# Optimization experiments

Measured on AMD Instinct MI355X. Metric: run time of the kernel, lower is better.

## Reference

```python
import jax, jax.numpy as jnp
import numpy as np

D = 256      # d_model
NH = 8       # heads
NL = 3       # layers
DFF = 1024   # ffn hidden
WIN = 64     # attention window
EPS = 1e-5


def _sin_pos_embed(L, d):
    # Sinusoidal positional embedding, matches _create_pos_embedding.
    pos = jnp.arange(L, dtype=jnp.float32)[:, None]
    div = jnp.exp(jnp.arange(0, d, 2, dtype=jnp.float32) * (-np.log(10000.0) / d))
    pe = jnp.zeros((L, d), jnp.float32)
    pe = pe.at[:, 0::2].set(jnp.sin(pos * div))
    pe = pe.at[:, 1::2].set(jnp.cos(pos * div))
    return pe  # [L, D]


def _layer_norm(x, scale, bias):
    m = jnp.mean(x, axis=-1, keepdims=True)
    v = jnp.mean(jnp.square(x - m), axis=-1, keepdims=True)
    return (x - m) * jax.lax.rsqrt(v + EPS) * scale + bias


def _mha(x, Wi, bi, Wo, bo):
    # x: [N, S, D]; Wi: [3D, D]; Wo: [D, D]. torch nn.MultiheadAttention semantics (eval, no dropout).
    N, S, _ = x.shape
    dh = D // NH
    qkv = x @ Wi.T + bi                       # [N, S, 3D]
    q, k, v = jnp.split(qkv, 3, axis=-1)
    q = q.reshape(N, S, NH, dh).transpose(0, 2, 1, 3) * (dh ** -0.5)
    k = k.reshape(N, S, NH, dh).transpose(0, 2, 1, 3)
    v = v.reshape(N, S, NH, dh).transpose(0, 2, 1, 3)
    attn = jax.nn.softmax(jnp.einsum('nhqd,nhkd->nhqk', q, k), axis=-1)
    out = jnp.einsum('nhqk,nhkd->nhqd', attn, v)
    out = out.transpose(0, 2, 1, 3).reshape(N, S, D)
    return out @ Wo.T + bo


def setup_inputs() -> dict:
    key = jax.random.key(0)
    ks = jax.random.split(key, 16)
    s = 0.02
    return {
        'features': jax.random.normal(ks[0], (32, D, 32, 32), jnp.float32),
        'in_proj_w': jax.random.normal(ks[1], (NL, 3 * D, D), jnp.float32) * s,
        'in_proj_b': jnp.zeros((NL, 3 * D), jnp.float32),
        'out_proj_w': jax.random.normal(ks[2], (NL, D, D), jnp.float32) * s,
        'out_proj_b': jnp.zeros((NL, D), jnp.float32),
        'w1': jax.random.normal(ks[3], (NL, DFF, D), jnp.float32) * s,
        'b1': jnp.zeros((NL, DFF), jnp.float32),
        'w2': jax.random.normal(ks[4], (NL, D, DFF), jnp.float32) * s,
        'b2': jnp.zeros((NL, D), jnp.float32),
        'ln1_s': jnp.ones((NL, D), jnp.float32),
        'ln1_b': jnp.zeros((NL, D), jnp.float32),
        'ln2_s': jnp.ones((NL, D), jnp.float32),
        'ln2_b': jnp.zeros((NL, D), jnp.float32),
        'fnorm_s': jnp.ones((D,), jnp.float32),
        'fnorm_b': jnp.zeros((D,), jnp.float32),
    }


def reference(features, in_proj_w, in_proj_b, out_proj_w, out_proj_b,
              w1, b1, w2, b2, ln1_s, ln1_b, ln2_s, ln2_b, fnorm_s, fnorm_b):
    B, C, H, W = features.shape
    L = H * W
    x = features.reshape(B, C, L).transpose(0, 2, 1)   # [B, L, D]
    x = x + _sin_pos_embed(L, D)[None]                 # L == 1024 == max_len, no interp
    nw = L // WIN                                      # non-overlapping windows
    for i in range(NL):
        # windowed self-attention: all windows batched in one MHA call
        xw = x.reshape(B * nw, WIN, D)
        att = _mha(xw, in_proj_w[i], in_proj_b[i], out_proj_w[i], out_proj_b[i])
        att = att.reshape(B, L, D)
        x = _layer_norm(x + att, ln1_s[i], ln1_b[i])
        h = jax.nn.gelu(x @ w1[i].T + b1[i], approximate=False) @ w2[i].T + b2[i]
        x = _layer_norm(x + h, ln2_s[i], ln2_b[i])
    x = _layer_norm(x, fnorm_s, fnorm_b)
    return x.transpose(0, 2, 1).reshape(B, C, H, W)
```

## Files before the change

kernel.cpp:

```cpp
#include <hip/hip_runtime.h>
#include <hip/hip_bf16.h>

#define BSZ 32
#define DM 256
#define LSEQ 1024
#define MTOK (BSZ * LSEQ)
#define NHEAD 8
#define DHEAD 32
#define WIN 64
#define DFF 1024
#define M8 ((size_t)MTOK * 8)

typedef short bf16x8 __attribute__((ext_vector_type(8)));
typedef float f32x4 __attribute__((ext_vector_type(4)));
typedef unsigned short u16x8 __attribute__((ext_vector_type(8)));

union BF { __hip_bfloat16 h; unsigned short u; };
__device__ __forceinline__ unsigned short f2bf(float f) { BF b; b.h = __float2bfloat16(f); return b.u; }
__device__ __forceinline__ float bf2f(unsigned short u) { return __uint_as_float((unsigned)u << 16); }

#define GLD_LDS16(gp, lp) __builtin_amdgcn_global_load_lds( \
    (const __attribute__((address_space(1))) void*)(gp),    \
    (__attribute__((address_space(3))) void*)(lp), 16, 0, 0)

__device__ __forceinline__ float gelu_fast(float x) {
    float t = x * (0.7978845608f + 0.0356774081f * x * x);
    return x / (1.0f + __expf(-2.0f * t));
}

__global__ __launch_bounds__(256) void cvt_kernel(
    const float* __restrict__ s, unsigned short* __restrict__ d,
    int N, int K, int nl)
{
    int K8 = K >> 3;
    int per = N * K8;
    int c = blockIdx.x * 256 + threadIdx.x;
    if (c >= per * nl) return;
    int layer = c / per, rem = c - layer * per;
    int n = rem / K8, kc = rem - n * K8;
    const float* sp = s + (size_t)layer * N * K + (size_t)n * K + kc * 8;
    float4 v0 = *(const float4*)sp, v1 = *(const float4*)(sp + 4);
    uint4 o;
    o.x = f2bf(v0.x) | ((unsigned)f2bf(v0.y) << 16);
    o.y = f2bf(v0.z) | ((unsigned)f2bf(v0.w) << 16);
    o.z = f2bf(v1.x) | ((unsigned)f2bf(v1.y) << 16);
    o.w = f2bf(v1.z) | ((unsigned)f2bf(v1.w) << 16);
    *(uint4*)(d + (size_t)layer * N * K + (size_t)kc * N * 8 + (size_t)n * 8) = o;
}

__global__ __launch_bounds__(256) void pe_kernel(float* __restrict__ PE)
{
    int l = blockIdx.x, c = threadIdx.x;
    int i2 = c & ~1;
    float div = expf(-9.210340371976184f * (float)i2 / 256.0f);
    float ang = (float)l * div;
    PE[l * DM + c] = (c & 1) ? cosf(ang) : sinf(ang);
}

__global__ __launch_bounds__(256) void embed_kernel(
    const float* __restrict__ F, const float* __restrict__ PE,
    float* __restrict__ Xf, unsigned short* __restrict__ Xb)
{
    __shared__ float tile[64][65];
    int b = blockIdx.z, l0 = blockIdx.y * 64, c0 = blockIdx.x * 64;
    int tid = threadIdx.x;
    int li = tid & 63, c4 = tid >> 6;
    #pragma unroll
    for (int it = 0; it < 16; ++it) {
        int c = c4 + it * 4;
        tile[c][li] = F[((size_t)(b * DM + c0 + c)) * LSEQ + l0 + li];
    }
    __syncthreads();
    int ci = tid & 63, l4 = tid >> 6;
    #pragma unroll
    for (int it = 0; it < 16; ++it) {
        int l = l4 + it * 4;
        float x = tile[ci][l] + PE[(l0 + l) * DM + c0 + ci];
        Xf[((size_t)b * LSEQ + l0 + l) * DM + c0 + ci] = x;
    }
    int ch = tid >> 5;
    int lx = tid & 31;
    #pragma unroll
    for (int rd = 0; rd < 2; ++rd) {
        int l = lx + rd * 32;
        unsigned short vs[8];
        #pragma unroll
        for (int e = 0; e < 8; ++e) {
            int c = ch * 8 + e;
            vs[e] = f2bf(tile[c][l] + PE[(l0 + l) * DM + c0 + c]);
        }
        uint4 o;
        o.x = vs[0] | ((unsigned)vs[1] << 16);
        o.y = vs[2] | ((unsigned)vs[3] << 16);
        o.z = vs[4] | ((unsigned)vs[5] << 16);
        o.w = vs[6] | ((unsigned)vs[7] << 16);
        *(uint4*)(Xb + ((size_t)((c0 >> 3) + ch)) * M8 +
                  (size_t)(b * LSEQ + l0 + l) * 8) = o;
    }
}

__global__ __launch_bounds__(256) void gemm_mfma_kernel(
    const unsigned short* __restrict__ A, const unsigned short* __restrict__ Bw,
    const float* __restrict__ bias, unsigned short* __restrict__ Cb,
    int M, int N, int K, int gelu)
{
    __shared__ __align__(16) char smem[17408];
    const int tid = threadIdx.x;
    const int lane = tid & 63, wave = tid >> 6;
    const int l15 = lane & 15, quad = lane >> 4;
    const int wm = (wave & 1) * 64, wn = (wave >> 1) * 64;
    const int m0 = blockIdx.x * 128, n0 = blockIdx.y * 128;
    const size_t Ma8 = (size_t)M * 8, Nb8 = (size_t)N * 8;
    const size_t astep = 4 * Ma8, bstep = 4 * Nb8;

    const unsigned short* ap[4];
    const unsigned short* bp[4];
    #pragma unroll
    for (int i = 0; i < 4; ++i)
        ap[i] = A + quad * Ma8 + (size_t)(m0 + wm + i * 16 + l15) * 8;
    #pragma unroll
    for (int j = 0; j < 4; ++j)
        bp[j] = Bw + quad * Nb8 + (size_t)(n0 + wn + j * 16 + l15) * 8;

    f32x4 acc[4][4] = {};
    bf16x8 aA[4], bA[4], aB[4], bB[4];
    #pragma unroll
    for (int i = 0; i < 4; ++i) aA[i] = *(const bf16x8*)(ap[i]);
    #pragma unroll
    for (int j = 0; j < 4; ++j) bA[j] = *(const bf16x8*)(bp[j]);

    const int iters = K >> 5;
    for (int t = 0; t < iters; t += 2) {
        size_t o1 = (size_t)(t + 1);
        #pragma unroll
        for (int i = 0; i < 4; ++i) aB[i] = *(const bf16x8*)(ap[i] + o1 * astep);
        #pragma unroll
        for (int j = 0; j < 4; ++j) bB[j] = *(const bf16x8*)(bp[j] + o1 * bstep);
        #pragma unroll
        for (int i = 0; i < 4; ++i)
            #pragma unroll
            for (int j = 0; j < 4; ++j)
                acc[i][j] = __builtin_amdgcn_mfma_f32_16x16x32_bf16(
                    aA[i], bA[j], acc[i][j], 0, 0, 0);
        size_t o2 = (size_t)((t + 2 < iters) ? t + 2 : iters - 1);
        #pragma unroll
        for (int i = 0; i < 4; ++i) aA[i] = *(const bf16x8*)(ap[i] + o2 * astep);
        #pragma unroll
        for (int j = 0; j < 4; ++j) bA[j] = *(const bf16x8*)(bp[j] + o2 * bstep);
        #pragma unroll
        for (int i = 0; i < 4; ++i)
            #pragma unroll
            for (int j = 0; j < 4; ++j)
                acc[i][j] = __builtin_amdgcn_mfma_f32_16x16x32_bf16(
                    aB[i], bB[j], acc[i][j], 0, 0, 0);
    }

    float* Es = (float*)(smem + wave * 4352);
    const int r16 = lane >> 2;
    const int cg  = (lane & 3) * 16;
    #pragma unroll
    for (int i = 0; i < 4; ++i) {
        #pragma unroll
        for (int j = 0; j < 4; ++j)
            #pragma unroll
            for (int r = 0; r < 4; ++r)
                Es[(quad * 4 + r) * 68 + j * 16 + l15] = acc[i][j][r];
        asm volatile("s_waitcnt lgkmcnt(0)" ::: "memory");

        int m = m0 + wm + i * 16 + r16;
        int nb = n0 + wn + cg;
        float v[16];
        #pragma unroll
        for (int c = 0; c < 4; ++c) {
            f32x4 t = *(const f32x4*)&Es[r16 * 68 + cg + c * 4];
            v[c * 4 + 0] = t[0]; v[c * 4 + 1] = t[1];
            v[c * 4 + 2] = t[2]; v[c * 4 + 3] = t[3];
        }
        #pragma unroll
        for (int c = 0; c < 4; ++c) {
            float4 bb = *(const float4*)(bias + nb + c * 4);
            v[c * 4 + 0] += bb.x; v[c * 4 + 1] += bb.y;
            v[c * 4 + 2] += bb.z; v[c * 4 + 3] += bb.w;
        }
        if (gelu) {
            #pragma unroll
            for (int e = 0; e < 16; ++e) v[e] = gelu_fast(v[e]);
        }
        size_t gb = ((size_t)(nb >> 3)) * Ma8 + (size_t)m * 8;
        #pragma unroll
        for (int c = 0; c < 2; ++c) {
            uint4 o;
            o.x = f2bf(v[c * 8 + 0]) | ((unsigned)f2bf(v[c * 8 + 1]) << 16);
            o.y = f2bf(v[c * 8 + 2]) | ((unsigned)f2bf(v[c * 8 + 3]) << 16);
            o.z = f2bf(v[c * 8 + 4]) | ((unsigned)f2bf(v[c * 8 + 5]) << 16);
            o.w = f2bf(v[c * 8 + 6]) | ((unsigned)f2bf(v[c * 8 + 7]) << 16);
            *(uint4*)(Cb + gb + (size_t)c * Ma8) = o;
        }
        asm volatile("" ::: "memory");
    }
}

__global__ __launch_bounds__(256) void gemm_ln_kernel(
    const unsigned short* __restrict__ A, const unsigned short* __restrict__ Bw,
    const float* __restrict__ bias, const float* __restrict__ resid,
    const float* __restrict__ lns, const float* __restrict__ lnb,
    float* __restrict__ Xf, unsigned short* __restrict__ Xb, int K)
{
    __shared__ __align__(16) char smem[17408];
    __shared__ float Ss[256], Sq[256];
    const int tid = threadIdx.x;
    const int lane = tid & 63, wave = tid >> 6;
    const int l15 = lane & 15, quad = lane >> 4;
    const int wn = wave * 64;
    const int m0 = blockIdx.x * 64;
    const size_t Nb8 = (size_t)DM * 8;
    const size_t astep = 4 * M8, bstep = 4 * Nb8;

    const unsigned short* ap[4];
    const unsigned short* bp[4];
    #pragma unroll
    for (int i = 0; i < 4; ++i)
        ap[i] = A + quad * M8 + (size_t)(m0 + i * 16 + l15) * 8;
    #pragma unroll
    for (int j = 0; j < 4; ++j)
        bp[j] = Bw + quad * Nb8 + (size_t)(wn + j * 16 + l15) * 8;

    f32x4 acc[4][4] = {};
    bf16x8 aA[4], bA[4], aB[4], bB[4];
    #pragma unroll
    for (int i = 0; i < 4; ++i) aA[i] = *(const bf16x8*)(ap[i]);
    #pragma unroll
    for (int j = 0; j < 4; ++j) bA[j] = *(const bf16x8*)(bp[j]);

    const int iters = K >> 5;
    for (int t = 0; t < iters; t += 2) {
        size_t o1 = (size_t)(t + 1);
        #pragma unroll
        for (int i = 0; i < 4; ++i) aB[i] = *(const bf16x8*)(ap[i] + o1 * astep);
        #pragma unroll
        for (int j = 0; j < 4; ++j) bB[j] = *(const bf16x8*)(bp[j] + o1 * bstep);
        #pragma unroll
        for (int i = 0; i < 4; ++i)
            #pragma unroll
            for (int j = 0; j < 4; ++j)
                acc[i][j] = __builtin_amdgcn_mfma_f32_16x16x32_bf16(
                    aA[i], bA[j], acc[i][j], 0, 0, 0);
        size_t o2 = (size_t)((t + 2 < iters) ? t + 2 : iters - 1);
        #pragma unroll
        for (int i = 0; i < 4; ++i) aA[i] = *(const bf16x8*)(ap[i] + o2 * astep);
        #pragma unroll
        for (int j = 0; j < 4; ++j) bA[j] = *(const bf16x8*)(bp[j] + o2 * bstep);
        #pragma unroll
        for (int i = 0; i < 4; ++i)
            #pragma unroll
            for (int j = 0; j < 4; ++j)
                acc[i][j] = __builtin_amdgcn_mfma_f32_16x16x32_bf16(
                    aB[i], bB[j], acc[i][j], 0, 0, 0);
    }

    float bj[4], scj[4], bbj[4];
    #pragma unroll
    for (int j = 0; j < 4; ++j) {
        int col = wn + j * 16 + l15;
        bj[j] = bias[col]; scj[j] = lns[col]; bbj[j] = lnb[col];
    }
    #pragma unroll
    for (int i = 0; i < 4; ++i)
        #pragma unroll
        for (int r = 0; r < 4; ++r) {
            const float* rp = resid + (size_t)(m0 + i * 16 + quad * 4 + r) * DM + wn;
            #pragma unroll
            for (int j = 0; j < 4; ++j)
                acc[i][j][r] += bj[j] + rp[j * 16 + l15];
        }

    #pragma unroll
    for (int i = 0; i < 4; ++i)
        #pragma unroll
        for (int r = 0; r < 4; ++r) {
            float s = 0.f, q = 0.f;
            #pragma unroll
            for (int j = 0; j < 4; ++j) {
                float x = acc[i][j][r];
                s += x; q = fmaf(x, x, q);
            }
            #pragma unroll
            for (int off = 1; off < 16; off <<= 1) {
                s += __shfl_xor(s, off);
                q += __shfl_xor(q, off);
            }
            if (l15 == 0) {
                int row = i * 16 + quad * 4 + r;
                Ss[wave * 64 + row] = s;
                Sq[wave * 64 + row] = q;
            }
        }
    __syncthreads();
    #pragma unroll
    for (int i = 0; i < 4; ++i)
        #pragma unroll
        for (int r = 0; r < 4; ++r) {
            int row = i * 16 + quad * 4 + r;
            float s = Ss[row] + Ss[64 + row] + Ss[128 + row] + Ss[192 + row];
            float q = Sq[row] + Sq[64 + row] + Sq[128 + row] + Sq[192 + row];
            float mean = s * (1.0f / 256.0f);
            float var  = q * (1.0f / 256.0f) - mean * mean;
            float rinv = rsqrtf(var + 1e-5f);
            #pragma unroll
            for (int j = 0; j < 4; ++j)
                acc[i][j][r] = (acc[i][j][r] - mean) * rinv * scj[j] + bbj[j];
        }

    float* Es = (float*)(smem + wave * 4352);
    const int r16 = lane >> 2;
    const int cg  = (lane & 3) * 16;
    #pragma unroll
    for (int i = 0; i < 4; ++i) {
        #pragma unroll
        for (int j = 0; j < 4; ++j)
            #pragma unroll
            for (int r = 0; r < 4; ++r)
                Es[(quad * 4 + r) * 68 + j * 16 + l15] = acc[i][j][r];
        asm volatile("s_waitcnt lgkmcnt(0)" ::: "memory");

        int m = m0 + i * 16 + r16;
        float v[16];
        #pragma unroll
        for (int c = 0; c < 4; ++c) {
            f32x4 t = *(const f32x4*)&Es[r16 * 68 + cg + c * 4];
            v[c * 4 + 0] = t[0]; v[c * 4 + 1] = t[1];
            v[c * 4 + 2] = t[2]; v[c * 4 + 3] = t[3];
        }
        size_t gf = (size_t)m * DM + wn + cg;
        #pragma unroll
        for (int c = 0; c < 4; ++c) {
            float4 o = { v[c * 4 + 0], v[c * 4 + 1], v[c * 4 + 2], v[c * 4 + 3] };
            *(float4*)(Xf + gf + c * 4) = o;
        }
        size_t gb = ((size_t)((wn + cg) >> 3)) * M8 + (size_t)m * 8;
        #pragma unroll
        for (int c = 0; c < 2; ++c) {
            uint4 o;
            o.x = f2bf(v[c * 8 + 0]) | ((unsigned)f2bf(v[c * 8 + 1]) << 16);
            o.y = f2bf(v[c * 8 + 2]) | ((unsigned)f2bf(v[c * 8 + 3]) << 16);
            o.z = f2bf(v[c * 8 + 4]) | ((unsigned)f2bf(v[c * 8 + 5]) << 16);
            o.w = f2bf(v[c * 8 + 6]) | ((unsigned)f2bf(v[c * 8 + 7]) << 16);
            *(uint4*)(Xb + gb + (size_t)c * M8) = o;
        }
        asm volatile("" ::: "memory");
    }
}

__global__ __launch_bounds__(64) void attn_mfma_kernel(
    const unsigned short* __restrict__ QKV, unsigned short* __restrict__ ATT)
{
    __shared__ __align__(16) char smem[22016];
    unsigned short* Qs = (unsigned short*)smem;
    unsigned short* Ks = (unsigned short*)(smem + 4096);
    unsigned short* VT = (unsigned short*)(smem + 8192);
    unsigned short* Ps = (unsigned short*)(smem + 12800);
    float*          Po = (float*)(smem + 12800);

    const int wg = blockIdx.x, h = blockIdx.y;
    const int base = wg * WIN;
    const int lane = threadIdx.x;
    const int l15 = lane & 15, quad = lane >> 4;
    const float scale = 0.17677669529663687f;

    #pragma unroll
    for (int dc = 0; dc < 4; ++dc) {
        GLD_LDS16(QKV + ((size_t)(h * 4 + dc)) * M8 + (size_t)(base + lane) * 8,
                  Qs + dc * 512 + (size_t)lane * 8);
        GLD_LDS16(QKV + ((size_t)(32 + h * 4 + dc)) * M8 + (size_t)(base + lane) * 8,
                  Ks + dc * 512 + (size_t)lane * 8);
    }
    u16x8 vv[4];
    #pragma unroll
    for (int cc = 0; cc < 4; ++cc)
        vv[cc] = *(const u16x8*)(QKV + ((size_t)(64 + h * 4 + cc)) * M8 +
                                 (size_t)(base + lane) * 8);
    #pragma unroll
    for (int cc = 0; cc < 4; ++cc)
        #pragma unroll
        for (int e = 0; e < 8; ++e)
            VT[(cc * 8 + e) * 72 + lane] = vv[cc][e];
    __syncthreads();

    const f32x4 zero4 = {0.f, 0.f, 0.f, 0.f};
    bf16x8 aq[4], bk[4];
    #pragma unroll
    for (int i = 0; i < 4; ++i)
        aq[i] = *(const bf16x8*)(Qs + quad * 512 + (i * 16 + l15) * 8);
    #pragma unroll
    for (int j = 0; j < 4; ++j)
        bk[j] = *(const bf16x8*)(Ks + quad * 512 + (j * 16 + l15) * 8);
    f32x4 S[4][4];
    #pragma unroll
    for (int i = 0; i < 4; ++i)
        #pragma unroll
        for (int j = 0; j < 4; ++j)
            S[i][j] = __builtin_amdgcn_mfma_f32_16x16x32_bf16(aq[i], bk[j], zero4, 0, 0, 0);

    float mx[4][4], sum[4][4];
    #pragma unroll
    for (int i = 0; i < 4; ++i)
        #pragma unroll
        for (int r = 0; r < 4; ++r) {
            float m0 = -1e30f;
            #pragma unroll
            for (int j = 0; j < 4; ++j) {
                S[i][j][r] *= scale;
                m0 = fmaxf(m0, S[i][j][r]);
            }
            mx[i][r] = m0;
        }
    #pragma unroll
    for (int off = 1; off < 16; off <<= 1)
        #pragma unroll
        for (int i = 0; i < 4; ++i)
            #pragma unroll
            for (int r = 0; r < 4; ++r)
                mx[i][r] = fmaxf(mx[i][r], __shfl_xor(mx[i][r], off));
    #pragma unroll
    for (int i = 0; i < 4; ++i)
        #pragma unroll
        for (int r = 0; r < 4; ++r) {
            float s0 = 0.f;
            #pragma unroll
            for (int j = 0; j < 4; ++j) {
                float e = __expf(S[i][j][r] - mx[i][r]);
                S[i][j][r] = e;
                s0 += e;
            }
            sum[i][r] = s0;
        }
    #pragma unroll
    for (int off = 1; off < 16; off <<= 1)
        #pragma unroll
        for (int i = 0; i < 4; ++i)
            #pragma unroll
            for (int r = 0; r < 4; ++r)
                sum[i][r] += __shfl_xor(sum[i][r], off);

    #pragma unroll
    for (int i = 0; i < 4; ++i)
        #pragma unroll
        for (int r = 0; r < 4; ++r) {
            float inv = 1.0f / sum[i][r];
            #pragma unroll
            for (int j = 0; j < 4; ++j)
                Ps[(i * 16 + quad * 4 + r) * 72 + j * 16 + l15] =
                    f2bf(S[i][j][r] * inv);
        }
    asm volatile("s_waitcnt lgkmcnt(0)" ::: "memory");

    bf16x8 ap0[4], ap1[4], bv0[2], bv1[2];
    #pragma unroll
    for (int i = 0; i < 4; ++i) {
        ap0[i] = *(const bf16x8*)(Ps + (i * 16 + l15) * 72 + quad * 8);
        ap1[i] = *(const bf16x8*)(Ps + (i * 16 + l15) * 72 + 32 + quad * 8);
    }
    #pragma unroll
    for (int jd = 0; jd < 2; ++jd) {
        bv0[jd] = *(const bf16x8*)(VT + (jd * 16 + l15) * 72 + quad * 8);
        bv1[jd] = *(const bf16x8*)(VT + (jd * 16 + l15) * 72 + 32 + quad * 8);
    }
    f32x4 O[4][2];
    #pragma unroll
    for (int i = 0; i < 4; ++i)
        #pragma unroll
        for (int jd = 0; jd < 2; ++jd) {
            f32x4 t = __builtin_amdgcn_mfma_f32_16x16x32_bf16(ap0[i], bv0[jd], zero4, 0, 0, 0);
            O[i][jd] = __builtin_amdgcn_mfma_f32_16x16x32_bf16(ap1[i], bv1[jd], t, 0, 0, 0);
        }
    asm volatile("s_waitcnt lgkmcnt(0)" ::: "memory");

    #pragma unroll
    for (int i = 0; i < 4; ++i)
        #pragma unroll
        for (int jd = 0; jd < 2; ++jd)
            #pragma unroll
            for (int r = 0; r < 4; ++r)
                Po[(i * 16 + quad * 4 + r) * 36 + jd * 16 + l15] = O[i][jd][r];
    asm volatile("s_waitcnt lgkmcnt(0)" ::: "memory");

    #pragma unroll
    for (int g = 0; g < 4; ++g) {
        f32x4 t0 = *(const f32x4*)(Po + lane * 36 + g * 8);
        f32x4 t1 = *(const f32x4*)(Po + lane * 36 + g * 8 + 4);
        uint4 w;
        w.x = f2bf(t0[0]) | ((unsigned)f2bf(t0[1]) << 16);
        w.y = f2bf(t0[2]) | ((unsigned)f2bf(t0[3]) << 16);
        w.z = f2bf(t1[0]) | ((unsigned)f2bf(t1[1]) << 16);
        w.w = f2bf(t1[2]) | ((unsigned)f2bf(t1[3]) << 16);
        *(uint4*)(ATT + ((size_t)(h * 4 + g)) * M8 + (size_t)(base + lane) * 8) = w;
    }
}

__global__ __launch_bounds__(256) void out_ln_kernel(
    const float* __restrict__ Xf, const float* __restrict__ sc,
    const float* __restrict__ bi, float* __restrict__ out)
{
    __shared__ float tile[64][257];
    __shared__ float mean_s[64], rinv_s[64];
    int b = blockIdx.y, l0 = blockIdx.x * 64;
    int tid = threadIdx.x, wave = tid >> 6, lane = tid & 63;
    int c = lane * 4;
    #pragma unroll
    for (int it = 0; it < 16; ++it) {
        int tl = wave * 16 + it;
        float4 v = *(const float4*)(Xf + ((size_t)(b * LSEQ + l0 + tl)) * DM + c);
        *(float4*)&tile[tl][c] = v;
        float sm = v.x + v.y + v.z + v.w;
        float sq = v.x * v.x + v.y * v.y + v.z * v.z + v.w * v.w;
        #pragma unroll
        for (int off = 32; off > 0; off >>= 1) {
            sm += __shfl_down(sm, off);
            sq += __shfl_down(sq, off);
        }
        if (lane == 0) {
            float mean = sm * (1.0f / 256.0f);
            float var  = sq * (1.0f / 256.0f) - mean * mean;
            mean_s[tl] = mean;
            rinv_s[tl] = rsqrtf(var + 1e-5f);
        }
    }
    __syncthreads();
    int lout = tid & 63, crow = tid >> 6;
    #pragma unroll
    for (int ct = 0; ct < 4; ++ct) {
        int c0 = ct * 64;
        #pragma unroll
        for (int it = 0; it < 16; ++it) {
            int cc = c0 + crow + it * 4;
            float v = tile[lout][cc];
            out[((size_t)(b * DM + cc)) * LSEQ + l0 + lout] =
                (v - mean_s[lout]) * rinv_s[lout] * sc[cc] + bi[cc];
        }
    }
}

extern "C" void kernel_launch(void* const* d_in, const int* in_sizes, int n_in,
                              void* d_out, int out_size, void* d_ws, size_t ws_size,
                              hipStream_t stream)
{
    const float* F   = (const float*)d_in[0];
    const float* Wi  = (const float*)d_in[1];
    const float* Bi  = (const float*)d_in[2];
    const float* Wo  = (const float*)d_in[3];
    const float* Bo  = (const float*)d_in[4];
    const float* W1  = (const float*)d_in[5];
    const float* B1  = (const float*)d_in[6];
    const float* W2  = (const float*)d_in[7];
    const float* B2  = (const float*)d_in[8];
    const float* L1s = (const float*)d_in[9];
    const float* L1b = (const float*)d_in[10];
    const float* L2s = (const float*)d_in[11];
    const float* L2b = (const float*)d_in[12];
    const float* Fs  = (const float*)d_in[13];
    const float* Fb  = (const float*)d_in[14];

    char* w = (char*)d_ws;
    float*          Xf   = (float*)w;
    unsigned short* QKVb = (unsigned short*)(w + 33554432);
    unsigned short* Hb   = (unsigned short*)(w + 83886080);
    unsigned short* Xb   = (unsigned short*)(w + 150994944);
    unsigned short* ATTb = (unsigned short*)(w + 167772160);
    unsigned short* WB   = (unsigned short*)(w + 184549376);
    float*          PE   = (float*)(w + 189267968);
    unsigned short* Wib  = WB;
    unsigned short* Wob  = WB + 589824;
    unsigned short* W1b  = WB + 786432;
    unsigned short* W2b  = WB + 1572864;

    cvt_kernel<<<(3 * 768 * 32 + 255) / 256, 256, 0, stream>>>(Wi, Wib, 768, 256, 3);
    cvt_kernel<<<(3 * 256 * 32 + 255) / 256, 256, 0, stream>>>(Wo, Wob, 256, 256, 3);
    cvt_kernel<<<(3 * 1024 * 32 + 255) / 256, 256, 0, stream>>>(W1, W1b, 1024, 256, 3);
    cvt_kernel<<<(3 * 256 * 128 + 255) / 256, 256, 0, stream>>>(W2, W2b, 256, 1024, 3);
    pe_kernel<<<LSEQ, 256, 0, stream>>>(PE);
    embed_kernel<<<dim3(DM / 64, LSEQ / 64, BSZ), 256, 0, stream>>>(F, PE, Xf, Xb);

    for (int i = 0; i < 3; ++i) {
        gemm_mfma_kernel<<<dim3(MTOK / 128, 768 / 128), 256, 0, stream>>>(
            Xb, Wib + (size_t)i * 196608, Bi + i * 768, QKVb, MTOK, 768, DM, 0);
        attn_mfma_kernel<<<dim3(BSZ * (LSEQ / WIN), NHEAD), 64, 0, stream>>>(QKVb, ATTb);
        gemm_ln_kernel<<<MTOK / 64, 256, 0, stream>>>(
            ATTb, Wob + (size_t)i * 65536, Bo + i * DM, Xf,
            L1s + i * DM, L1b + i * DM, Xf, Xb, DM);
        gemm_mfma_kernel<<<dim3(MTOK / 128, DFF / 128), 256, 0, stream>>>(
            Xb, W1b + (size_t)i * 262144, B1 + i * DFF, Hb, MTOK, DFF, DM, 1);
        gemm_ln_kernel<<<MTOK / 64, 256, 0, stream>>>(
            Hb, W2b + (size_t)i * 262144, B2 + i * DM, Xf,
            L2s + i * DM, L2b + i * DM, Xf, Xb, DFF);
    }

    out_ln_kernel<<<dim3(LSEQ / 64, BSZ), 256, 0, stream>>>(
        Xf, Fs, Fb, (float*)d_out);
}
```

Baseline: 648.6 us.

## Fuse FFN up-projection, GELU, down-projection and LayerNorm into one kernel

Replaces the separate W1 GEMM (with GELU) and the W2 GEMM+LayerNorm kernels with one fused kernel per 64-token tile. The 1024-wide hidden activation is built in chunks of 256 in shared memory, so it is never written to or read back from global memory. The change also swaps bf16 conversion for a cheaper add-and-shift packer, which rounds ties differently and does not handle NaN specially, and hoists the bias loads out of the QKV GEMM epilogue. The trade-offs are more shared memory per block, which limits occupancy, and W2 operands loaded straight from global memory without software prefetch.

After: 663.9 us. 2.4% more time.

```diff
diff --git a/kernel.cpp b/kernel.cpp
--- a/kernel.cpp
+++ b/kernel.cpp
@@ -18,6 +18,11 @@
 union BF { __hip_bfloat16 h; unsigned short u; };
 __device__ __forceinline__ unsigned short f2bf(float f) { BF b; b.h = __float2bfloat16(f); return b.u; }
 __device__ __forceinline__ float bf2f(unsigned short u) { return __uint_as_float((unsigned)u << 16); }
+__device__ __forceinline__ unsigned pk2bf(float a, float b) {
+    unsigned ua = __float_as_uint(a) + 0x8000u;
+    unsigned ub = __float_as_uint(b) + 0x8000u;
+    return (ua >> 16) | (ub & 0xffff0000u);
+}
 
 #define GLD_LDS16(gp, lp) __builtin_amdgcn_global_load_lds( \
     (const __attribute__((address_space(1))) void*)(gp),    \
@@ -40,11 +45,8 @@
     int n = rem / K8, kc = rem - n * K8;
     const float* sp = s + (size_t)layer * N * K + (size_t)n * K + kc * 8;
     float4 v0 = *(const float4*)sp, v1 = *(const float4*)(sp + 4);
-    uint4 o;
-    o.x = f2bf(v0.x) | ((unsigned)f2bf(v0.y) << 16);
-    o.y = f2bf(v0.z) | ((unsigned)f2bf(v0.w) << 16);
-    o.z = f2bf(v1.x) | ((unsigned)f2bf(v1.y) << 16);
-    o.w = f2bf(v1.z) | ((unsigned)f2bf(v1.w) << 16);
+    uint4 o = { pk2bf(v0.x, v0.y), pk2bf(v0.z, v0.w),
+                pk2bf(v1.x, v1.y), pk2bf(v1.z, v1.w) };
     *(uint4*)(d + (size_t)layer * N * K + (size_t)kc * N * 8 + (size_t)n * 8) = o;
 }
 
@@ -83,17 +85,14 @@
     #pragma unroll
     for (int rd = 0; rd < 2; ++rd) {
         int l = lx + rd * 32;
-        unsigned short vs[8];
+        float vs[8];
         #pragma unroll
         for (int e = 0; e < 8; ++e) {
             int c = ch * 8 + e;
-            vs[e] = f2bf(tile[c][l] + PE[(l0 + l) * DM + c0 + c]);
-        }
-        uint4 o;
-        o.x = vs[0] | ((unsigned)vs[1] << 16);
-        o.y = vs[2] | ((unsigned)vs[3] << 16);
-        o.z = vs[4] | ((unsigned)vs[5] << 16);
-        o.w = vs[6] | ((unsigned)vs[7] << 16);
+            vs[e] = tile[c][l] + PE[(l0 + l) * DM + c0 + c];
+        }
+        uint4 o = { pk2bf(vs[0], vs[1]), pk2bf(vs[2], vs[3]),
+                    pk2bf(vs[4], vs[5]), pk2bf(vs[6], vs[7]) };
         *(uint4*)(Xb + ((size_t)((c0 >> 3) + ch)) * M8 +
                   (size_t)(b * LSEQ + l0 + l) * 8) = o;
     }
@@ -102,7 +101,7 @@
 __global__ __launch_bounds__(256) void gemm_mfma_kernel(
     const unsigned short* __restrict__ A, const unsigned short* __restrict__ Bw,
     const float* __restrict__ bias, unsigned short* __restrict__ Cb,
-    int M, int N, int K, int gelu)
+    int M, int N, int K)
 {
     __shared__ __align__(16) char smem[17408];
     const int tid = threadIdx.x;
@@ -158,6 +157,14 @@
     float* Es = (float*)(smem + wave * 4352);
     const int r16 = lane >> 2;
     const int cg  = (lane & 3) * 16;
+    const int nb = n0 + wn + cg;
+    float bb[16];
+    #pragma unroll
+    for (int c = 0; c < 4; ++c) {
+        float4 b4 = *(const float4*)(bias + nb + c * 4);
+        bb[c * 4 + 0] = b4.x; bb[c * 4 + 1] = b4.y;
+        bb[c * 4 + 2] = b4.z; bb[c * 4 + 3] = b4.w;
+    }
     #pragma unroll
     for (int i = 0; i < 4; ++i) {
         #pragma unroll
@@ -168,32 +175,20 @@
         asm volatile("s_waitcnt lgkmcnt(0)" ::: "memory");
 
         int m = m0 + wm + i * 16 + r16;
-        int nb = n0 + wn + cg;
         float v[16];
         #pragma unroll
         for (int c = 0; c < 4; ++c) {
             f32x4 t = *(const f32x4*)&Es[r16 * 68 + cg + c * 4];
-            v[c * 4 + 0] = t[0]; v[c * 4 + 1] = t[1];
-            v[c * 4 + 2] = t[2]; v[c * 4 + 3] = t[3];
-        }
-        #pragma unroll
-        for (int c = 0; c < 4; ++c) {
-            float4 bb = *(const float4*)(bias + nb + c * 4);
-            v[c * 4 + 0] += bb.x; v[c * 4 + 1] += bb.y;
-            v[c * 4 + 2] += bb.z; v[c * 4 + 3] += bb.w;
-        }
-        if (gelu) {
-            #pragma unroll
-            for (int e = 0; e < 16; ++e) v[e] = gelu_fast(v[e]);
+            v[c * 4 + 0] = t[0] + bb[c * 4 + 0];
+            v[c * 4 + 1] = t[1] + bb[c * 4 + 1];
+            v[c * 4 + 2] = t[2] + bb[c * 4 + 2];
+            v[c * 4 + 3] = t[3] + bb[c * 4 + 3];
         }
         size_t gb = ((size_t)(nb >> 3)) * Ma8 + (size_t)m * 8;
         #pragma unroll
         for (int c = 0; c < 2; ++c) {
-            uint4 o;
-            o.x = f2bf(v[c * 8 + 0]) | ((unsigned)f2bf(v[c * 8 + 1]) << 16);
-            o.y = f2bf(v[c * 8 + 2]) | ((unsigned)f2bf(v[c * 8 + 3]) << 16);
-            o.z = f2bf(v[c * 8 + 4]) | ((unsigned)f2bf(v[c * 8 + 5]) << 16);
-            o.w = f2bf(v[c * 8 + 6]) | ((unsigned)f2bf(v[c * 8 + 7]) << 16);
+            uint4 o = { pk2bf(v[c*8+0], v[c*8+1]), pk2bf(v[c*8+2], v[c*8+3]),
+                        pk2bf(v[c*8+4], v[c*8+5]), pk2bf(v[c*8+6], v[c*8+7]) };
             *(uint4*)(Cb + gb + (size_t)c * Ma8) = o;
         }
         asm volatile("" ::: "memory");
@@ -340,12 +335,213 @@
         size_t gb = ((size_t)((wn + cg) >> 3)) * M8 + (size_t)m * 8;
         #pragma unroll
         for (int c = 0; c < 2; ++c) {
-            uint4 o;
-            o.x = f2bf(v[c * 8 + 0]) | ((unsigned)f2bf(v[c * 8 + 1]) << 16);
-            o.y = f2bf(v[c * 8 + 2]) | ((unsigned)f2bf(v[c * 8 + 3]) << 16);
-            o.z = f2bf(v[c * 8 + 4]) | ((unsigned)f2bf(v[c * 8 + 5]) << 16);
-            o.w = f2bf(v[c * 8 + 6]) | ((unsigned)f2bf(v[c * 8 + 7]) << 16);
+            uint4 o = { pk2bf(v[c*8+0], v[c*8+1]), pk2bf(v[c*8+2], v[c*8+3]),
+                        pk2bf(v[c*8+4], v[c*8+5]), pk2bf(v[c*8+6], v[c*8+7]) };
             *(uint4*)(Xb + gb + (size_t)c * M8) = o;
+        }
+        asm volatile("" ::: "memory");
+    }
+}
+
+__global__ __launch_bounds__(256, 2) void ffn_fused_kernel(
+    const unsigned short* __restrict__ Xb, const unsigned short* __restrict__ W1b,
+    const float* __restrict__ b1, const unsigned short* __restrict__ W2b,
+    const float* __restrict__ b2, const float* __restrict__ resid,
+    const float* __restrict__ lns, const float* __restrict__ lnb,
+    float* __restrict__ XfOut, unsigned short* __restrict__ XbOut)
+{
+    __shared__ __align__(16) char smem[32768 + 17408 + 2048];
+    unsigned short* Hs = (unsigned short*)smem;
+    float* Ss = (float*)(smem + 32768 + 17408);
+    float* Sq = Ss + 256;
+
+    const int tid = threadIdx.x;
+    const int lane = tid & 63, wave = tid >> 6;
+    const int l15 = lane & 15, quad = lane >> 4;
+    const int wn = wave * 64;
+    const int m0 = blockIdx.x * 64;
+    const size_t w1step = 4 * (size_t)DFF * 8;
+    const size_t astep  = 4 * M8;
+    float* Es = (float*)(smem + 32768 + wave * 4352);
+    const int r16 = lane >> 2;
+    const int cg  = (lane & 3) * 16;
+
+    const unsigned short* ap[4];
+    #pragma unroll
+    for (int i = 0; i < 4; ++i)
+        ap[i] = Xb + quad * M8 + (size_t)(m0 + i * 16 + l15) * 8;
+
+    f32x4 acc2[4][4] = {};
+
+    for (int g = 0; g < 4; ++g) {
+        const int hbase = g * 256 + wn;
+        const unsigned short* bp[4];
+        #pragma unroll
+        for (int j = 0; j < 4; ++j)
+            bp[j] = W1b + quad * ((size_t)DFF * 8) + (size_t)(hbase + j * 16 + l15) * 8;
+
+        f32x4 acc1[4][4] = {};
+        bf16x8 aA[4], bA[4], aB[4], bB[4];
+        #pragma unroll
+        for (int i = 0; i < 4; ++i) aA[i] = *(const bf16x8*)(ap[i]);
+        #pragma unroll
+        for (int j = 0; j < 4; ++j) bA[j] = *(const bf16x8*)(bp[j]);
+        for (int t = 0; t < 8; t += 2) {
+            size_t o1 = (size_t)(t + 1);
+            #pragma unroll
+            for (int i = 0; i < 4; ++i) aB[i] = *(const bf16x8*)(ap[i] + o1 * astep);
+            #pragma unroll
+            for (int j = 0; j < 4; ++j) bB[j] = *(const bf16x8*)(bp[j] + o1 * w1step);
+            #pragma unroll
+            for (int i = 0; i < 4; ++i)
+                #pragma unroll
+                for (int j = 0; j < 4; ++j)
+                    acc1[i][j] = __builtin_amdgcn_mfma_f32_16x16x32_bf16(
+                        aA[i], bA[j], acc1[i][j], 0, 0, 0);
+            size_t o2 = (size_t)((t + 2 < 8) ? t + 2 : 7);
+            #pragma unroll
+            for (int i = 0; i < 4; ++i) aA[i] = *(const bf16x8*)(ap[i] + o2 * astep);
+            #pragma unroll
+            for (int j = 0; j < 4; ++j) bA[j] = *(const bf16x8*)(bp[j] + o2 * w1step);
+            #pragma unroll
+            for (int i = 0; i < 4; ++i)
+                #pragma unroll
+                for (int j = 0; j < 4; ++j)
+                    acc1[i][j] = __builtin_amdgcn_mfma_f32_16x16x32_bf16(
+                        aB[i], bB[j], acc1[i][j], 0, 0, 0);
+        }
+        float b1j[4];
+        #pragma unroll
+        for (int j = 0; j < 4; ++j) b1j[j] = b1[hbase + j * 16 + l15];
+        #pragma unroll
+        for (int i = 0; i < 4; ++i) {
+            #pragma unroll
+            for (int j = 0; j < 4; ++j)
+                #pragma unroll
+                for (int r = 0; r < 4; ++r)
+                    Es[(quad * 4 + r) * 68 + j * 16 + l15] =
+                        gelu_fast(acc1[i][j][r] + b1j[j]);
+            asm volatile("s_waitcnt lgkmcnt(0)" ::: "memory");
+            int m = i * 16 + r16;
+            float v[16];
+            #pragma unroll
+            for (int c = 0; c < 4; ++c) {
+                f32x4 t = *(const f32x4*)&Es[r16 * 68 + cg + c * 4];
+                v[c * 4 + 0] = t[0]; v[c * 4 + 1] = t[1];
+                v[c * 4 + 2] = t[2]; v[c * 4 + 3] = t[3];
+            }
+            int kcl = (wn + cg) >> 3;
+            #pragma unroll
+            for (int c = 0; c < 2; ++c) {
+                uint4 o = { pk2bf(v[c*8+0], v[c*8+1]), pk2bf(v[c*8+2], v[c*8+3]),
+                            pk2bf(v[c*8+4], v[c*8+5]), pk2bf(v[c*8+6], v[c*8+7]) };
+                *(uint4*)(Hs + (size_t)(kcl + c) * 512 + (size_t)m * 8) = o;
+            }
+            asm volatile("" ::: "memory");
+        }
+        __syncthreads();
+
+        #pragma unroll 2
+        for (int tl = 0; tl < 8; ++tl) {
+            int kcl = quad + 4 * tl;
+            bf16x8 a2[4], bw2[4];
+            #pragma unroll
+            for (int i = 0; i < 4; ++i)
+                a2[i] = *(const bf16x8*)(Hs + (size_t)kcl * 512 + (size_t)(i * 16 + l15) * 8);
+            size_t kc2 = (size_t)(g * 32 + kcl);
+            #pragma unroll
+            for (int j = 0; j < 4; ++j)
+                bw2[j] = *(const bf16x8*)(W2b + kc2 * ((size_t)DM * 8) +
+                                          (size_t)(wn + j * 16 + l15) * 8);
+            #pragma unroll
+            for (int i = 0; i < 4; ++i)
+                #pragma unroll
+                for (int j = 0; j < 4; ++j)
+                    acc2[i][j] = __builtin_amdgcn_mfma_f32_16x16x32_bf16(
+                        a2[i], bw2[j], acc2[i][j], 0, 0, 0);
+        }
+        __syncthreads();
+    }
+
+    float bj[4], scj[4], bbj[4];
+    #pragma unroll
+    for (int j = 0; j < 4; ++j) {
+        int col = wn + j * 16 + l15;
+        bj[j] = b2[col]; scj[j] = lns[col]; bbj[j] = lnb[col];
+    }
+    #pragma unroll
+    for (int i = 0; i < 4; ++i)
+        #pragma unroll
+        for (int r = 0; r < 4; ++r) {
+            const float* rp = resid + (size_t)(m0 + i * 16 + quad * 4 + r) * DM + wn;
+            #pragma unroll
+            for (int j = 0; j < 4; ++j)
+                acc2[i][j][r] += bj[j] + rp[j * 16 + l15];
+        }
+    #pragma unroll
+    for (int i = 0; i < 4; ++i)
+        #pragma unroll
+        for (int r = 0; r < 4; ++r) {
+            float s = 0.f, q = 0.f;
+            #pragma unroll
+            for (int j = 0; j < 4; ++j) {
+                float x = acc2[i][j][r];
+                s += x; q = fmaf(x, x, q);
+            }
+            #pragma unroll
+            for (int off = 1; off < 16; off <<= 1) {
+                s += __shfl_xor(s, off);
+                q += __shfl_xor(q, off);
+            }
+            if (l15 == 0) {
+                int row = i * 16 + quad * 4 + r;
+                Ss[wave * 64 + row] = s;
+                Sq[wave * 64 + row] = q;
+            }
+        }
+    __syncthreads();
+    #pragma unroll
+    for (int i = 0; i < 4; ++i)
+        #pragma unroll
+        for (int r = 0; r < 4; ++r) {
+            int row = i * 16 + quad * 4 + r;
+            float s = Ss[row] + Ss[64 + row] + Ss[128 + row] + Ss[192 + row];
+            float q = Sq[row] + Sq[64 + row] + Sq[128 + row] + Sq[192 + row];
+            float mean = s * (1.0f / 256.0f);
+            float var  = q * (1.0f / 256.0f) - mean * mean;
+            float rinv = rsqrtf(var + 1e-5f);
+            #pragma unroll
+            for (int j = 0; j < 4; ++j)
+                acc2[i][j][r] = (acc2[i][j][r] - mean) * rinv * scj[j] + bbj[j];
+        }
+    #pragma unroll
+    for (int i = 0; i < 4; ++i) {
+        #pragma unroll
+        for (int j = 0; j < 4; ++j)
+            #pragma unroll
+            for (int r = 0; r < 4; ++r)
+                Es[(quad * 4 + r) * 68 + j * 16 + l15] = acc2[i][j][r];
+        asm volatile("s_waitcnt lgkmcnt(0)" ::: "memory");
+        int m = m0 + i * 16 + r16;
+        float v[16];
+        #pragma unroll
+        for (int c = 0; c < 4; ++c) {
+            f32x4 t = *(const f32x4*)&Es[r16 * 68 + cg + c * 4];
+            v[c * 4 + 0] = t[0]; v[c * 4 + 1] = t[1];
+            v[c * 4 + 2] = t[2]; v[c * 4 + 3] = t[3];
+        }
+        size_t gf = (size_t)m * DM + wn + cg;
+        #pragma unroll
+        for (int c = 0; c < 4; ++c) {
+            float4 o = { v[c * 4 + 0], v[c * 4 + 1], v[c * 4 + 2], v[c * 4 + 3] };
+            *(float4*)(XfOut + gf + c * 4) = o;
+        }
+        size_t gb = ((size_t)((wn + cg) >> 3)) * M8 + (size_t)m * 8;
+        #pragma unroll
+        for (int c = 0; c < 2; ++c) {
+            uint4 o = { pk2bf(v[c*8+0], v[c*8+1]), pk2bf(v[c*8+2], v[c*8+3]),
+                        pk2bf(v[c*8+4], v[c*8+5]), pk2bf(v[c*8+6], v[c*8+7]) };
+            *(uint4*)(XbOut + gb + (size_t)c * M8) = o;
         }
         asm volatile("" ::: "memory");
     }
@@ -488,11 +684,8 @@
     for (int g = 0; g < 4; ++g) {
         f32x4 t0 = *(const f32x4*)(Po + lane * 36 + g * 8);
         f32x4 t1 = *(const f32x4*)(Po + lane * 36 + g * 8 + 4);
-        uint4 w;
-        w.x = f2bf(t0[0]) | ((unsigned)f2bf(t0[1]) << 16);
-        w.y = f2bf(t0[2]) | ((unsigned)f2bf(t0[3]) << 16);
-        w.z = f2bf(t1[0]) | ((unsigned)f2bf(t1[1]) << 16);
-        w.w = f2bf(t1[2]) | ((unsigned)f2bf(t1[3]) << 16);
+        uint4 w = { pk2bf(t0[0], t0[1]), pk2bf(t0[2], t0[3]),
+                    pk2bf(t1[0], t1[1]), pk2bf(t1[2], t1[3]) };
         *(uint4*)(ATT + ((size_t)(h * 4 + g)) * M8 + (size_t)(base + lane) * 8) = w;
     }
 }
@@ -563,7 +756,6 @@
     char* w = (char*)d_ws;
     float*          Xf   = (float*)w;
     unsigned short* QKVb = (unsigned short*)(w + 33554432);
-    unsigned short* Hb   = (unsigned short*)(w + 83886080);
     unsigned short* Xb   = (unsigned short*)(w + 150994944);
     unsigned short* ATTb = (unsigned short*)(w + 167772160);
     unsigned short* WB   = (unsigned short*)(w + 184549376);
@@ -582,16 +774,15 @@
 
     for (int i = 0; i < 3; ++i) {
         gemm_mfma_kernel<<<dim3(MTOK / 128, 768 / 128), 256, 0, stream>>>(
-            Xb, Wib + (size_t)i * 196608, Bi + i * 768, QKVb, MTOK, 768, DM, 0);
+            Xb, Wib + (size_t)i * 196608, Bi + i * 768, QKVb, MTOK, 768, DM);
         attn_mfma_kernel<<<dim3(BSZ * (LSEQ / WIN), NHEAD), 64, 0, stream>>>(QKVb, ATTb);
         gemm_ln_kernel<<<MTOK / 64, 256, 0, stream>>>(
             ATTb, Wob + (size_t)i * 65536, Bo + i * DM, Xf,
             L1s + i * DM, L1b + i * DM, Xf, Xb, DM);
-        gemm_mfma_kernel<<<dim3(MTOK / 128, DFF / 128), 256, 0, stream>>>(
-            Xb, W1b + (size_t)i * 262144, B1 + i * DFF, Hb, MTOK, DFF, DM, 1);
-        gemm_ln_kernel<<<MTOK / 64, 256, 0, stream>>>(
-            Hb, W2b + (size_t)i * 262144, B2 + i * DM, Xf,
-            L2s + i * DM, L2b + i * DM, Xf, Xb, DFF);
+        ffn_fused_kernel<<<MTOK / 64, 256, 0, stream>>>(
+            Xb, W1b + (size_t)i * 262144, B1 + i * DFF,
+            W2b + (size_t)i * 262144, B2 + i * DM, Xf,
+            L2s + i * DM, L2b + i * DM, Xf, Xb);
     }
 
     out_ln_kernel<<<dim3(LSEQ / 64, BSZ), 256, 0, stream>>>(
```
